# Optimization experiments

Measured on AMD Instinct MI355X. Metric: run time of the kernel, lower is better.

Reference implementation:

```python
import jax, jax.numpy as jnp
import numpy as np

B, N, X, Y, W1, W2 = 1, 6, 16, 16, 8, 8
DIM, HEADS, DH = 128, 4, 32
INNER = HEADS * DH
EPS = 1e-5


def setup_inputs() -> dict:
    key = jax.random.key(0)
    ks = jax.random.split(key, 8)
    s = 0.02
    shp = (B, N, X, Y, W1, W2, DIM)
    return {
        "q": jax.random.normal(ks[0], shp, jnp.float32),
        "k": jax.random.normal(ks[1], shp, jnp.float32),
        "v": jax.random.normal(ks[2], shp, jnp.float32),
        "ln_q_g": jnp.ones((DIM,), jnp.float32), "ln_q_b": jnp.zeros((DIM,), jnp.float32),
        "ln_k_g": jnp.ones((DIM,), jnp.float32), "ln_k_b": jnp.zeros((DIM,), jnp.float32),
        "ln_v_g": jnp.ones((DIM,), jnp.float32), "ln_v_b": jnp.zeros((DIM,), jnp.float32),
        "Wq": jax.random.normal(ks[3], (DIM, INNER), jnp.float32) * s, "bq": jnp.zeros((INNER,), jnp.float32),
        "Wk": jax.random.normal(ks[4], (DIM, INNER), jnp.float32) * s, "bk": jnp.zeros((INNER,), jnp.float32),
        "Wv": jax.random.normal(ks[5], (DIM, INNER), jnp.float32) * s, "bv": jnp.zeros((INNER,), jnp.float32),
        "Wp": jax.random.normal(ks[6], (INNER, DIM), jnp.float32) * s, "bp": jnp.zeros((DIM,), jnp.float32),
    }


def _layernorm(x, g, b):
    m = x.mean(-1, keepdims=True)
    v = x.var(-1, keepdims=True)
    return (x - m) / jnp.sqrt(v + EPS) * g + b


def _to_windows(t):
    # 'b n x y w1 w2 d -> b (x y) (n w1 w2) d'
    b, n, x, y, w1, w2, d = t.shape
    t = jnp.transpose(t, (0, 2, 3, 1, 4, 5, 6))
    return t.reshape(b, x * y, n * w1 * w2, d)


def _norm_proj_heads(t, g, bb, W, bias):
    # norm + linear, then 'b l t (h d) -> b h l t d'
    t = _layernorm(t, g, bb) @ W + bias
    b, L, T, _ = t.shape
    t = t.reshape(b, L, T, HEADS, DH)
    return jnp.transpose(t, (0, 3, 1, 2, 4))


def reference(q, k, v, ln_q_g, ln_q_b, ln_k_g, ln_k_b, ln_v_g, ln_v_b,
              Wq, bq, Wk, bk, Wv, bv, Wp, bp):
    qh = _norm_proj_heads(_to_windows(q), ln_q_g, ln_q_b, Wq, bq)  # (b,h,L,Q,dh)
    kh = _norm_proj_heads(_to_windows(k), ln_k_g, ln_k_b, Wk, bk)
    vh = _norm_proj_heads(_to_windows(v), ln_v_g, ln_v_b, Wv, bv)
    scale = DH ** -0.5
    dot = scale * jnp.einsum('bhlqd,bhlkd->bhlqk', qh, kh)  # (b,h,L,Q,K)
    att = jax.nn.softmax(dot, axis=-1)
    a = jnp.einsum('bhlqk,bhlkd->bhlqd', att, vh)  # (b,h,L,Q,dh)
    # merge heads: 'b h l q d -> b l q (h d)'
    a = jnp.transpose(a, (0, 2, 3, 1, 4)).reshape(B, X * Y, N * W1 * W2, INNER)
    z = a @ Wp + bp  # (b, L, Q, DIM)
    # 'b (x y) (n w1 w2) d -> b n x y w1 w2 d' then mean over n
    z = z.reshape(B, X, Y, N, W1, W2, DIM)
    z = jnp.transpose(z, (0, 3, 1, 2, 4, 5, 6)).mean(axis=1)
    return z  # (b, x, y, w1, w2, DIM)
```

## Files before the change

### kernel.cpp

```cpp
#include <hip/hip_runtime.h>
#include <hip/hip_bf16.h>

typedef unsigned short u16;
typedef __attribute__((ext_vector_type(8))) short b16x8;
typedef __attribute__((ext_vector_type(4))) float f32x4;

__device__ __forceinline__ u16 f2bf(float f) {
    union { float f; unsigned int u; } v; v.f = f;
    unsigned int u = v.u;
    return (u16)((u + 0x7FFFu + ((u >> 16) & 1u)) >> 16);
}

__global__ __launch_bounds__(256) void k_pack_w(const float* __restrict__ w0,
                                                const float* __restrict__ w1,
                                                const float* __restrict__ w2,
                                                const float* __restrict__ w3,
                                                u16* __restrict__ dstbase) {
    const float* src = (blockIdx.x == 0) ? w0 : (blockIdx.x == 1) ? w1
                     : (blockIdx.x == 2) ? w2 : w3;
    u16* dst = dstbase + blockIdx.x * 16384;
    for (int i = threadIdx.x; i < 16384; i += 256) {
        int k = i >> 7, n = i & 127;
        dst[n * 128 + k] = f2bf(src[i]);
    }
}

struct K1Args {
    const float* x[3];
    const float* lng[3];
    const float* lnb[3];
    const float* bias[3];
    u16* out[3];
};

__global__ __launch_bounds__(256) void k_ln_proj(K1Args a, const u16* __restrict__ wt) {
    __shared__ u16 sW[16384];
    __shared__ u16 sA[8192];
    const int tid = threadIdx.x;
    const int tensor = blockIdx.y;

    const u16* wsrc = wt + tensor * 16384;
#pragma unroll
    for (int it = 0; it < 8; ++it) {
        int e = (it * 256 + tid) << 3;
        int n = e >> 7, k0 = e & 127;
        b16x8 v = *(const b16x8*)(wsrc + e);
        *(b16x8*)(sW + n * 128 + (((k0 >> 3) ^ (n & 7)) << 3)) = v;
    }

    const int r = tid >> 2, sub = tid & 3;
    const long long tt = (long long)blockIdx.x * 64 + r;
    const int l = (int)(tt / 384), ti = (int)(tt % 384);
    const int nn = ti >> 6, w = ti & 63;
    const float* rowp = a.x[tensor] + ((long long)(nn * 16384 + l * 64 + w)) * 128 + sub * 32;
    float v[32];
    float s = 0.f, s2 = 0.f;
#pragma unroll
    for (int j = 0; j < 32; j += 4) {
        float4 f = *(const float4*)(rowp + j);
        v[j] = f.x; v[j + 1] = f.y; v[j + 2] = f.z; v[j + 3] = f.w;
        s  += (f.x + f.y) + (f.z + f.w);
        s2 += (f.x * f.x + f.y * f.y) + (f.z * f.z + f.w * f.w);
    }
    s  += __shfl_xor(s, 1);  s  += __shfl_xor(s, 2);
    s2 += __shfl_xor(s2, 1); s2 += __shfl_xor(s2, 2);
    const float mean = s * (1.f / 128.f);
    const float rstd = rsqrtf(s2 * (1.f / 128.f) - mean * mean + 1e-5f);
    const float* gp = a.lng[tensor];
    const float* bbp = a.lnb[tensor];
#pragma unroll
    for (int j = 0; j < 32; j += 8) {
        int k0 = sub * 32 + j;
        b16x8 tv;
#pragma unroll
        for (int q = 0; q < 8; ++q) {
            int k = k0 + q;
            tv[q] = (short)f2bf((v[j + q] - mean) * rstd * gp[k] + bbp[k]);
        }
        *(b16x8*)(sA + r * 128 + (((k0 >> 3) ^ (r & 7)) << 3)) = tv;
    }
    __syncthreads();

    const int wv = tid >> 6, lane = tid & 63, lr = lane & 15, lg = lane >> 4;
    f32x4 acc[8];
#pragma unroll
    for (int i = 0; i < 8; ++i) acc[i] = (f32x4){0.f, 0.f, 0.f, 0.f};
    const int rowA = wv * 16 + lr;
#pragma unroll
    for (int kt = 0; kt < 4; ++kt) {
        const int ch = lg + 4 * kt;
        b16x8 af = *(const b16x8*)(sA + rowA * 128 + ((ch ^ (rowA & 7)) << 3));
#pragma unroll
        for (int nt = 0; nt < 8; ++nt) {
            const int nc = nt * 16 + lr;
            b16x8 bf = *(const b16x8*)(sW + nc * 128 + ((ch ^ (nc & 7)) << 3));
            acc[nt] = __builtin_amdgcn_mfma_f32_16x16x32_bf16(af, bf, acc[nt], 0, 0, 0);
        }
    }
    const float scale = (tensor == 0) ? 0.17677669529663687f : 1.0f;
    u16* outp = a.out[tensor];
    const float* biasp = a.bias[tensor];
    const long long ttb = (long long)blockIdx.x * 64 + wv * 16;
#pragma unroll
    for (int nt = 0; nt < 8; ++nt) {
        const int col = nt * 16 + lr;
        const float bb = biasp[col];
#pragma unroll
        for (int rg = 0; rg < 4; ++rg) {
            const long long trow = ttb + lg * 4 + rg;
            outp[trow * 128 + col] = f2bf((acc[nt][rg] + bb) * scale);
        }
    }
}

__global__ __launch_bounds__(256) void k_attn(const u16* __restrict__ qh,
                                              const u16* __restrict__ kh,
                                              const u16* __restrict__ vh,
                                              u16* __restrict__ ah) {
    __shared__ u16 sK[384 * 40];
    __shared__ u16 sVt[32 * 392];
    __shared__ u16 sP[4 * 16 * 192];
    const int tid = threadIdx.x;
    const int l = blockIdx.x, h = blockIdx.y;
    const long long base = ((long long)l * 384) * 128 + h * 32;

#pragma unroll
    for (int it = 0; it < 6; ++it) {
        int idx = it * 256 + tid;
        int t = idx >> 2, c = (idx & 3) << 3;
        b16x8 kv = *(const b16x8*)(kh + base + (long long)t * 128 + c);
        *(b16x8*)(sK + t * 40 + c) = kv;
        b16x8 vv = *(const b16x8*)(vh + base + (long long)t * 128 + c);
#pragma unroll
        for (int q = 0; q < 8; ++q) sVt[(c + q) * 392 + t] = (u16)vv[q];
    }
    __syncthreads();

    const int wv = tid >> 6, lane = tid & 63, lr = lane & 15, lg = lane >> 4;
    u16* myP = sP + wv * 16 * 192;

    for (int qt = wv; qt < 24; qt += 4) {
        b16x8 qf = *(const b16x8*)(qh + base + (long long)(qt * 16 + lr) * 128 + lg * 8);
        f32x4 sacc[24];
#pragma unroll
        for (int kt = 0; kt < 24; ++kt) {
            b16x8 kf = *(const b16x8*)(sK + (kt * 16 + lr) * 40 + lg * 8);
            sacc[kt] = __builtin_amdgcn_mfma_f32_16x16x32_bf16(
                qf, kf, (f32x4){0.f, 0.f, 0.f, 0.f}, 0, 0, 0);
        }
        float sm[4];
#pragma unroll
        for (int rg = 0; rg < 4; ++rg) {
            float m = sacc[0][rg];
#pragma unroll
            for (int kt = 1; kt < 24; ++kt) m = fmaxf(m, sacc[kt][rg]);
            m = fmaxf(m, __shfl_xor(m, 1));
            m = fmaxf(m, __shfl_xor(m, 2));
            m = fmaxf(m, __shfl_xor(m, 4));
            m = fmaxf(m, __shfl_xor(m, 8));
            float ss = 0.f;
#pragma unroll
            for (int kt = 0; kt < 24; ++kt) {
                float e = __expf(sacc[kt][rg] - m);
                sacc[kt][rg] = e;
                ss += e;
            }
            ss += __shfl_xor(ss, 1); ss += __shfl_xor(ss, 2);
            ss += __shfl_xor(ss, 4); ss += __shfl_xor(ss, 8);
            sm[rg] = ss;
        }
        f32x4 pacc[2];
        pacc[0] = (f32x4){0.f, 0.f, 0.f, 0.f};
        pacc[1] = (f32x4){0.f, 0.f, 0.f, 0.f};
#pragma unroll
        for (int half = 0; half < 2; ++half) {
#pragma unroll
            for (int kt = 0; kt < 12; ++kt) {
#pragma unroll
                for (int rg = 0; rg < 4; ++rg) {
                    int q = lg * 4 + rg;
                    int tl = kt * 16 + lr;
                    int ch = (tl >> 3) ^ (q & 7);
                    myP[q * 192 + ch * 8 + (tl & 7)] = f2bf(sacc[half * 12 + kt][rg]);
                }
            }
#pragma unroll
            for (int k2 = 0; k2 < 6; ++k2) {
                int ch = (4 * k2 + lg) ^ (lr & 7);
                b16x8 pf = *(const b16x8*)(myP + lr * 192 + ch * 8);
#pragma unroll
                for (int nt = 0; nt < 2; ++nt) {
                    b16x8 vf = *(const b16x8*)(sVt + (nt * 16 + lr) * 392 +
                                               half * 192 + k2 * 32 + lg * 8);
                    pacc[nt] = __builtin_amdgcn_mfma_f32_16x16x32_bf16(pf, vf, pacc[nt], 0, 0, 0);
                }
            }
        }
#pragma unroll
        for (int nt = 0; nt < 2; ++nt) {
#pragma unroll
            for (int rg = 0; rg < 4; ++rg) {
                float aa = pacc[nt][rg] / sm[rg];
                long long trow = (long long)(qt * 16 + lg * 4 + rg);
                ah[base + trow * 128 + nt * 16 + lr] = f2bf(aa);
            }
        }
    }
}

__global__ __launch_bounds__(256) void k_proj_mean(const u16* __restrict__ ah,
                                                   const u16* __restrict__ wtp,
                                                   const float* __restrict__ bp,
                                                   float* __restrict__ out) {
    __shared__ u16 sW[16384];
    const int tid = threadIdx.x;
    const int l = blockIdx.x;
#pragma unroll
    for (int it = 0; it < 8; ++it) {
        int e = (it * 256 + tid) << 3;
        int n = e >> 7, k0 = e & 127;
        b16x8 v = *(const b16x8*)(wtp + e);
        *(b16x8*)(sW + n * 128 + (((k0 >> 3) ^ (n & 7)) << 3)) = v;
    }
    __syncthreads();
    const int wv = tid >> 6, lane = tid & 63, lr = lane & 15, lg = lane >> 4;
    f32x4 acc[8];
#pragma unroll
    for (int i = 0; i < 8; ++i) acc[i] = (f32x4){0.f, 0.f, 0.f, 0.f};
#pragma unroll
    for (int nn = 0; nn < 6; ++nn) {
        const int mt = wv + nn * 4;
        const long long rowb = ((long long)l * 384 + mt * 16 + lr) * 128;
#pragma unroll
        for (int kt = 0; kt < 4; ++kt) {
            b16x8 af = *(const b16x8*)(ah + rowb + kt * 32 + lg * 8);
            const int ch = lg + 4 * kt;
#pragma unroll
            for (int nt = 0; nt < 8; ++nt) {
                const int nc = nt * 16 + lr;
                b16x8 bf = *(const b16x8*)(sW + nc * 128 + ((ch ^ (nc & 7)) << 3));
                acc[nt] = __builtin_amdgcn_mfma_f32_16x16x32_bf16(af, bf, acc[nt], 0, 0, 0);
            }
        }
    }
#pragma unroll
    for (int nt = 0; nt < 8; ++nt) {
        const int col = nt * 16 + lr;
        const float bb = bp[col];
#pragma unroll
        for (int rg = 0; rg < 4; ++rg) {
            const int wrow = wv * 16 + lg * 4 + rg;
            out[((long long)l * 64 + wrow) * 128 + col] = acc[nt][rg] * (1.0f / 6.0f) + bb;
        }
    }
}

extern "C" void kernel_launch(void* const* d_in, const int* in_sizes, int n_in,
                              void* d_out, int out_size, void* d_ws, size_t ws_size,
                              hipStream_t stream) {
    (void)in_sizes; (void)n_in; (void)out_size; (void)ws_size;
    const float* q      = (const float*)d_in[0];
    const float* k      = (const float*)d_in[1];
    const float* v      = (const float*)d_in[2];
    const float* ln_q_g = (const float*)d_in[3];
    const float* ln_q_b = (const float*)d_in[4];
    const float* ln_k_g = (const float*)d_in[5];
    const float* ln_k_b = (const float*)d_in[6];
    const float* ln_v_g = (const float*)d_in[7];
    const float* ln_v_b = (const float*)d_in[8];
    const float* Wq     = (const float*)d_in[9];
    const float* bq     = (const float*)d_in[10];
    const float* Wk     = (const float*)d_in[11];
    const float* bk     = (const float*)d_in[12];
    const float* Wv     = (const float*)d_in[13];
    const float* bv     = (const float*)d_in[14];
    const float* Wp     = (const float*)d_in[15];
    const float* bp     = (const float*)d_in[16];
    float* out = (float*)d_out;

    u16* ws = (u16*)d_ws;
    const long long MATE = 98304LL * 128;
    u16* wQ  = ws;
    u16* wK  = ws + MATE;
    u16* wV  = ws + 2 * MATE;
    u16* wA  = ws + 3 * MATE;
    u16* wWt = ws + 4 * MATE;

    k_pack_w<<<4, 256, 0, stream>>>(Wq, Wk, Wv, Wp, wWt);

    K1Args args;
    args.x[0] = q;       args.x[1] = k;       args.x[2] = v;
    args.lng[0] = ln_q_g; args.lng[1] = ln_k_g; args.lng[2] = ln_v_g;
    args.lnb[0] = ln_q_b; args.lnb[1] = ln_k_b; args.lnb[2] = ln_v_b;
    args.bias[0] = bq;   args.bias[1] = bk;   args.bias[2] = bv;
    args.out[0] = wQ;    args.out[1] = wK;    args.out[2] = wV;
    k_ln_proj<<<dim3(1536, 3), 256, 0, stream>>>(args, wWt);

    k_attn<<<dim3(256, 4), 256, 0, stream>>>(wQ, wK, wV, wA);

    k_proj_mean<<<256, 256, 0, stream>>>(wA, wWt + 3 * 16384, bp, out);
}
```

Baseline: 336.8 us.

## Pre-swizzle weights, emit transposed V, stage outputs through LDS, widen blocks

```diff
diff --git a/kernel.cpp b/kernel.cpp
--- a/kernel.cpp
+++ b/kernel.cpp
@@ -16,12 +16,17 @@
                                                 const float* __restrict__ w2,
                                                 const float* __restrict__ w3,
                                                 u16* __restrict__ dstbase) {
-    const float* src = (blockIdx.x == 0) ? w0 : (blockIdx.x == 1) ? w1
-                     : (blockIdx.x == 2) ? w2 : w3;
-    u16* dst = dstbase + blockIdx.x * 16384;
-    for (int i = threadIdx.x; i < 16384; i += 256) {
+    const int b = blockIdx.x;
+    const int tensor = b >> 2;
+    const float* src = (tensor == 0) ? w0 : (tensor == 1) ? w1
+                     : (tensor == 2) ? w2 : w3;
+    u16* dst = dstbase + tensor * 16384;
+    const int i0 = (b & 3) * 4096;
+    for (int j = threadIdx.x; j < 4096; j += 256) {
+        int i = i0 + j;
         int k = i >> 7, n = i & 127;
-        dst[n * 128 + k] = f2bf(src[i]);
+        int kc = k >> 3, kr = k & 7;
+        dst[n * 128 + ((kc ^ (n & 7)) << 3) + kr] = f2bf(src[i]);
     }
 }
 
@@ -30,29 +35,30 @@
     const float* lng[3];
     const float* lnb[3];
     const float* bias[3];
-    u16* out[3];
+    u16* outQ; u16* outK; u16* outVt;
 };
 
-__global__ __launch_bounds__(256) void k_ln_proj(K1Args a, const u16* __restrict__ wt) {
+__global__ __launch_bounds__(512, 4) void k_ln_proj(K1Args a, const u16* __restrict__ wt) {
     __shared__ u16 sW[16384];
-    __shared__ u16 sA[8192];
+    __shared__ u16 sA[16384];
     const int tid = threadIdx.x;
     const int tensor = blockIdx.y;
+    const int wv = tid >> 6;
 
     const u16* wsrc = wt + tensor * 16384;
 #pragma unroll
-    for (int it = 0; it < 8; ++it) {
-        int e = (it * 256 + tid) << 3;
-        int n = e >> 7, k0 = e & 127;
-        b16x8 v = *(const b16x8*)(wsrc + e);
-        *(b16x8*)(sW + n * 128 + (((k0 >> 3) ^ (n & 7)) << 3)) = v;
+    for (int it = 0; it < 4; ++it) {
+        int e = (it * 512 + tid) << 3;
+        *(b16x8*)(sW + e) = *(const b16x8*)(wsrc + e);
     }
 
     const int r = tid >> 2, sub = tid & 3;
-    const long long tt = (long long)blockIdx.x * 64 + r;
-    const int l = (int)(tt / 384), ti = (int)(tt % 384);
+    const int token0 = blockIdx.x * 128;
+    const int l = token0 / 384;
+    const int tloc0 = token0 % 384;
+    const int ti = tloc0 + r;
     const int nn = ti >> 6, w = ti & 63;
-    const float* rowp = a.x[tensor] + ((long long)(nn * 16384 + l * 64 + w)) * 128 + sub * 32;
+    const float* rowp = a.x[tensor] + (size_t)(nn * 16384 + l * 64 + w) * 128 + sub * 32;
     float v[32];
     float s = 0.f, s2 = 0.f;
 #pragma unroll
@@ -81,14 +87,14 @@
     }
     __syncthreads();
 
-    const int wv = tid >> 6, lane = tid & 63, lr = lane & 15, lg = lane >> 4;
+    const int lane = tid & 63, lr = lane & 15, lg = lane >> 4;
     f32x4 acc[8];
 #pragma unroll
     for (int i = 0; i < 8; ++i) acc[i] = (f32x4){0.f, 0.f, 0.f, 0.f};
     const int rowA = wv * 16 + lr;
 #pragma unroll
     for (int kt = 0; kt < 4; ++kt) {
-        const int ch = lg + 4 * kt;
+        const int ch = kt * 4 + lg;
         b16x8 af = *(const b16x8*)(sA + rowA * 128 + ((ch ^ (rowA & 7)) << 3));
 #pragma unroll
         for (int nt = 0; nt < 8; ++nt) {
@@ -97,54 +103,86 @@
             acc[nt] = __builtin_amdgcn_mfma_f32_16x16x32_bf16(af, bf, acc[nt], 0, 0, 0);
         }
     }
-    const float scale = (tensor == 0) ? 0.17677669529663687f : 1.0f;
-    u16* outp = a.out[tensor];
+
     const float* biasp = a.bias[tensor];
-    const long long ttb = (long long)blockIdx.x * 64 + wv * 16;
-#pragma unroll
-    for (int nt = 0; nt < 8; ++nt) {
-        const int col = nt * 16 + lr;
-        const float bb = biasp[col];
-#pragma unroll
-        for (int rg = 0; rg < 4; ++rg) {
-            const long long trow = ttb + lg * 4 + rg;
-            outp[trow * 128 + col] = f2bf((acc[nt][rg] + bb) * scale);
-        }
-    }
-}
-
-__global__ __launch_bounds__(256) void k_attn(const u16* __restrict__ qh,
-                                              const u16* __restrict__ kh,
-                                              const u16* __restrict__ vh,
-                                              u16* __restrict__ ah) {
-    __shared__ u16 sK[384 * 40];
-    __shared__ u16 sVt[32 * 392];
-    __shared__ u16 sP[4 * 16 * 192];
+    if (tensor != 2) {
+        const float scale = (tensor == 0) ? 0.17677669529663687f : 1.0f;
+        u16* outp = (tensor == 0) ? a.outQ : a.outK;
+#pragma unroll
+        for (int nt = 0; nt < 8; ++nt) {
+            const int col = nt * 16 + lr;
+            const float bb = biasp[col];
+#pragma unroll
+            for (int rg = 0; rg < 4; ++rg) {
+                const int rowl = wv * 16 + lg * 4 + rg;
+                float val = (acc[nt][rg] + bb) * scale;
+                int cch = col >> 3;
+                sA[rowl * 128 + ((cch ^ (rowl & 7)) << 3) + (col & 7)] = f2bf(val);
+            }
+        }
+        const int rrow = wv * 16 + (lane >> 2);
+#pragma unroll
+        for (int c = 0; c < 4; ++c) {
+            int colc = (lane & 3) + c * 4;
+            b16x8 val = *(const b16x8*)(sA + rrow * 128 + ((colc ^ (rrow & 7)) << 3));
+            *(b16x8*)(outp + (size_t)(token0 + rrow) * 128 + colc * 8) = val;
+        }
+    } else {
+        __syncthreads();
+#pragma unroll
+        for (int nt = 0; nt < 8; ++nt) {
+            const int col = nt * 16 + lr;
+            const float bb = biasp[col];
+#pragma unroll
+            for (int rg = 0; rg < 4; ++rg) {
+                const int trowl = wv * 16 + lg * 4 + rg;
+                float val = acc[nt][rg] + bb;
+                int tch = trowl >> 3;
+                sA[col * 128 + ((tch ^ (col & 7)) << 3) + (trowl & 7)] = f2bf(val);
+            }
+        }
+        __syncthreads();
+        const int f = tid >> 2;
+        const size_t vb = ((size_t)(l * 4 + (f >> 5)) * 32 + (f & 31)) * 384 + tloc0;
+#pragma unroll
+        for (int c = 0; c < 4; ++c) {
+            int tch = (tid & 3) + c * 4;
+            b16x8 val = *(const b16x8*)(sA + f * 128 + ((tch ^ (f & 7)) << 3));
+            *(b16x8*)(a.outVt + vb + tch * 8) = val;
+        }
+    }
+}
+
+__global__ __launch_bounds__(256, 3) void k_attn(const u16* __restrict__ qh,
+                                                 const u16* __restrict__ kh,
+                                                 const u16* __restrict__ vt,
+                                                 u16* __restrict__ ah) {
+    __shared__ u16 sK[384 * 32];
+    __shared__ u16 sP[4][16 * 104];
     const int tid = threadIdx.x;
     const int l = blockIdx.x, h = blockIdx.y;
-    const long long base = ((long long)l * 384) * 128 + h * 32;
+    const size_t baseQ = ((size_t)l * 384) * 128 + h * 32;
+    const size_t baseV = ((size_t)(l * 4 + h) * 32) * 384;
 
 #pragma unroll
     for (int it = 0; it < 6; ++it) {
         int idx = it * 256 + tid;
-        int t = idx >> 2, c = (idx & 3) << 3;
-        b16x8 kv = *(const b16x8*)(kh + base + (long long)t * 128 + c);
-        *(b16x8*)(sK + t * 40 + c) = kv;
-        b16x8 vv = *(const b16x8*)(vh + base + (long long)t * 128 + c);
-#pragma unroll
-        for (int q = 0; q < 8; ++q) sVt[(c + q) * 392 + t] = (u16)vv[q];
+        int t = idx >> 2, c = idx & 3;
+        b16x8 kv = *(const b16x8*)(kh + baseQ + (size_t)t * 128 + c * 8);
+        *(b16x8*)(sK + t * 32 + ((c ^ (t & 3)) << 3)) = kv;
     }
     __syncthreads();
 
     const int wv = tid >> 6, lane = tid & 63, lr = lane & 15, lg = lane >> 4;
-    u16* myP = sP + wv * 16 * 192;
+    u16* myP = sP[wv];
 
     for (int qt = wv; qt < 24; qt += 4) {
-        b16x8 qf = *(const b16x8*)(qh + base + (long long)(qt * 16 + lr) * 128 + lg * 8);
+        b16x8 qf = *(const b16x8*)(qh + baseQ + (size_t)(qt * 16 + lr) * 128 + lg * 8);
         f32x4 sacc[24];
 #pragma unroll
         for (int kt = 0; kt < 24; ++kt) {
-            b16x8 kf = *(const b16x8*)(sK + (kt * 16 + lr) * 40 + lg * 8);
+            const int t = kt * 16 + lr;
+            b16x8 kf = *(const b16x8*)(sK + t * 32 + ((lg ^ (t & 3)) << 3));
             sacc[kt] = __builtin_amdgcn_mfma_f32_16x16x32_bf16(
                 qf, kf, (f32x4){0.f, 0.f, 0.f, 0.f}, 0, 0, 0);
         }
@@ -173,25 +211,25 @@
         pacc[0] = (f32x4){0.f, 0.f, 0.f, 0.f};
         pacc[1] = (f32x4){0.f, 0.f, 0.f, 0.f};
 #pragma unroll
-        for (int half = 0; half < 2; ++half) {
-#pragma unroll
-            for (int kt = 0; kt < 12; ++kt) {
+        for (int chunk = 0; chunk < 4; ++chunk) {
+#pragma unroll
+            for (int kc = 0; kc < 6; ++kc) {
+                const int kt = chunk * 6 + kc;
 #pragma unroll
                 for (int rg = 0; rg < 4; ++rg) {
                     int q = lg * 4 + rg;
-                    int tl = kt * 16 + lr;
-                    int ch = (tl >> 3) ^ (q & 7);
-                    myP[q * 192 + ch * 8 + (tl & 7)] = f2bf(sacc[half * 12 + kt][rg]);
+                    int tl = kc * 16 + lr;
+                    myP[q * 104 + tl] = f2bf(sacc[kt][rg]);
                 }
             }
 #pragma unroll
-            for (int k2 = 0; k2 < 6; ++k2) {
-                int ch = (4 * k2 + lg) ^ (lr & 7);
-                b16x8 pf = *(const b16x8*)(myP + lr * 192 + ch * 8);
+            for (int k2 = 0; k2 < 3; ++k2) {
+                b16x8 pf = *(const b16x8*)(myP + lr * 104 + k2 * 32 + lg * 8);
 #pragma unroll
                 for (int nt = 0; nt < 2; ++nt) {
-                    b16x8 vf = *(const b16x8*)(sVt + (nt * 16 + lr) * 392 +
-                                               half * 192 + k2 * 32 + lg * 8);
+                    b16x8 vf = *(const b16x8*)(vt + baseV +
+                                               (size_t)(nt * 16 + lr) * 384 +
+                                               chunk * 96 + k2 * 32 + lg * 8);
                     pacc[nt] = __builtin_amdgcn_mfma_f32_16x16x32_bf16(pf, vf, pacc[nt], 0, 0, 0);
                 }
             }
@@ -201,56 +239,56 @@
 #pragma unroll
             for (int rg = 0; rg < 4; ++rg) {
                 float aa = pacc[nt][rg] / sm[rg];
-                long long trow = (long long)(qt * 16 + lg * 4 + rg);
-                ah[base + trow * 128 + nt * 16 + lr] = f2bf(aa);
-            }
-        }
-    }
-}
-
-__global__ __launch_bounds__(256) void k_proj_mean(const u16* __restrict__ ah,
-                                                   const u16* __restrict__ wtp,
-                                                   const float* __restrict__ bp,
-                                                   float* __restrict__ out) {
+                size_t trow = (size_t)(qt * 16 + lg * 4 + rg);
+                ah[baseQ + trow * 128 + nt * 16 + lr] = f2bf(aa);
+            }
+        }
+    }
+}
+
+__global__ __launch_bounds__(512, 2) void k_proj_mean(const u16* __restrict__ ah,
+                                                      const u16* __restrict__ wtp,
+                                                      const float* __restrict__ bp,
+                                                      float* __restrict__ out) {
     __shared__ u16 sW[16384];
     const int tid = threadIdx.x;
     const int l = blockIdx.x;
 #pragma unroll
-    for (int it = 0; it < 8; ++it) {
-        int e = (it * 256 + tid) << 3;
-        int n = e >> 7, k0 = e & 127;
-        b16x8 v = *(const b16x8*)(wtp + e);
-        *(b16x8*)(sW + n * 128 + (((k0 >> 3) ^ (n & 7)) << 3)) = v;
+    for (int it = 0; it < 4; ++it) {
+        int e = (it * 512 + tid) << 3;
+        *(b16x8*)(sW + e) = *(const b16x8*)(wtp + e);
     }
     __syncthreads();
-    const int wv = tid >> 6, lane = tid & 63, lr = lane & 15, lg = lane >> 4;
-    f32x4 acc[8];
-#pragma unroll
-    for (int i = 0; i < 8; ++i) acc[i] = (f32x4){0.f, 0.f, 0.f, 0.f};
+    const int wv8 = tid >> 6;
+    const int wm = wv8 >> 1, wn = wv8 & 1;
+    const int lane = tid & 63, lr = lane & 15, lg = lane >> 4;
+    f32x4 acc[4];
+#pragma unroll
+    for (int i = 0; i < 4; ++i) acc[i] = (f32x4){0.f, 0.f, 0.f, 0.f};
 #pragma unroll
     for (int nn = 0; nn < 6; ++nn) {
-        const int mt = wv + nn * 4;
-        const long long rowb = ((long long)l * 384 + mt * 16 + lr) * 128;
+        const int mt = wm + nn * 4;
+        const size_t rowb = ((size_t)l * 384 + mt * 16 + lr) * 128;
 #pragma unroll
         for (int kt = 0; kt < 4; ++kt) {
             b16x8 af = *(const b16x8*)(ah + rowb + kt * 32 + lg * 8);
-            const int ch = lg + 4 * kt;
-#pragma unroll
-            for (int nt = 0; nt < 8; ++nt) {
-                const int nc = nt * 16 + lr;
+            const int ch = kt * 4 + lg;
+#pragma unroll
+            for (int nt = 0; nt < 4; ++nt) {
+                const int nc = (wn * 4 + nt) * 16 + lr;
                 b16x8 bf = *(const b16x8*)(sW + nc * 128 + ((ch ^ (nc & 7)) << 3));
                 acc[nt] = __builtin_amdgcn_mfma_f32_16x16x32_bf16(af, bf, acc[nt], 0, 0, 0);
             }
         }
     }
 #pragma unroll
-    for (int nt = 0; nt < 8; ++nt) {
-        const int col = nt * 16 + lr;
+    for (int nt = 0; nt < 4; ++nt) {
+        const int col = (wn * 4 + nt) * 16 + lr;
         const float bb = bp[col];
 #pragma unroll
         for (int rg = 0; rg < 4; ++rg) {
-            const int wrow = wv * 16 + lg * 4 + rg;
-            out[((long long)l * 64 + wrow) * 128 + col] = acc[nt][rg] * (1.0f / 6.0f) + bb;
+            const int wrow = wm * 16 + lg * 4 + rg;
+            out[((size_t)l * 64 + wrow) * 128 + col] = acc[nt][rg] * (1.0f / 6.0f) + bb;
         }
     }
 }
@@ -282,21 +320,21 @@
     const long long MATE = 98304LL * 128;
     u16* wQ  = ws;
     u16* wK  = ws + MATE;
-    u16* wV  = ws + 2 * MATE;
+    u16* wVt = ws + 2 * MATE;
     u16* wA  = ws + 3 * MATE;
     u16* wWt = ws + 4 * MATE;
 
-    k_pack_w<<<4, 256, 0, stream>>>(Wq, Wk, Wv, Wp, wWt);
+    k_pack_w<<<16, 256, 0, stream>>>(Wq, Wk, Wv, Wp, wWt);
 
     K1Args args;
     args.x[0] = q;       args.x[1] = k;       args.x[2] = v;
     args.lng[0] = ln_q_g; args.lng[1] = ln_k_g; args.lng[2] = ln_v_g;
     args.lnb[0] = ln_q_b; args.lnb[1] = ln_k_b; args.lnb[2] = ln_v_b;
     args.bias[0] = bq;   args.bias[1] = bk;   args.bias[2] = bv;
-    args.out[0] = wQ;    args.out[1] = wK;    args.out[2] = wV;
-    k_ln_proj<<<dim3(1536, 3), 256, 0, stream>>>(args, wWt);
-
-    k_attn<<<dim3(256, 4), 256, 0, stream>>>(wQ, wK, wV, wA);
-
-    k_proj_mean<<<256, 256, 0, stream>>>(wA, wWt + 3 * 16384, bp, out);
-}
+    args.outQ = wQ;      args.outK = wK;      args.outVt = wVt;
+    k_ln_proj<<<dim3(768, 3), 512, 0, stream>>>(args, wWt);
+
+    k_attn<<<dim3(256, 4), 256, 0, stream>>>(wQ, wK, wVt, wA);
+
+    k_proj_mean<<<256, 512, 0, stream>>>(wA, wWt + 3 * 16384, bp, out);
+}
```

After: 349.9 us. +3.9%, slower.
